# Kernel optimization log

Hardware: AMD Instinct MI355X
Metric: run time of the kernel (lower is better)

## Reference

```python
import jax, jax.numpy as jnp
import numpy as np

B, T, D = 4, 2048, 1024
E, H, K = 8, 2048, 2  # n_expert, expert_dim, top_k


def setup_inputs() -> dict:
    key = jax.random.key(0)
    k1, k2, k3, k4 = jax.random.split(key, 4)
    x = jax.random.normal(k1, (B, T, D), jnp.float32)
    gate_w = jax.random.normal(k2, (D, E), jnp.float32) * 0.02          # Router gate (no bias)
    w1 = jax.random.normal(k3, (E, D, H), jnp.float32) * (1.0 / np.sqrt(D))  # per-expert first Linear
    w2 = jax.random.normal(k4, (E, H, D), jnp.float32) * (1.0 / np.sqrt(H))  # per-expert second Linear
    return {"x": x, "gate_w": gate_w, "w1": w1, "w2": w2}


def reference(x, gate_w, w1, w2):
    b, t, d = x.shape
    xf = x.reshape(-1, d)                                   # [N, D]
    n = xf.shape[0]
    n_expert = gate_w.shape[1]
    # Router
    logits = xf @ gate_w                                    # [N, E]
    probs = jax.nn.softmax(logits, axis=-1)
    topk_probs, topk_idx = jax.lax.top_k(probs, K)          # [N, K]
    topk_probs = topk_probs / jnp.sum(topk_probs, axis=-1, keepdims=True)
    # Dense compute of ALL experts (faithful to original), then gather top-k
    h = jax.nn.gelu(jnp.einsum('nd,edh->neh', xf, w1), approximate=False)  # [N, E, H]
    all_expert_out = jnp.einsum('neh,ehd->ned', h, w2)      # [N, E, D]
    selected = jnp.take_along_axis(all_expert_out, topk_idx[:, :, None], axis=1)  # [N, K, D]
    out = jnp.sum(topk_probs[:, :, None] * selected, axis=1)  # [N, D]  (dropout p=0 -> identity)
    # Load-balancing aux loss
    counts = jnp.zeros((n_expert,), jnp.float32).at[topk_idx.reshape(-1)].add(1.0)
    tokens_per_expert = counts / n
    mean_probs = jnp.mean(probs, axis=0)
    aux_loss = n_expert * jnp.sum(tokens_per_expert * mean_probs)
    return (out.reshape(b, t, d), aux_loss,
            probs.reshape(b, t, n_expert),
            topk_idx.reshape(b, t, K),
            topk_probs.reshape(b, t, K))
```

## Files before the change

### kernel.cpp

```cpp
#include <hip/hip_runtime.h>
#include <hip/hip_bf16.h>
#include <cstdint>

typedef unsigned short u16;
typedef unsigned int u32;
typedef short s16x8 __attribute__((ext_vector_type(8)));
typedef float f32x4 __attribute__((ext_vector_type(4)));

constexpr int NTOK = 8192;
constexpr int DDIM = 1024;
constexpr int NEXP = 8;
constexpr int HDIM = 2048;
constexpr int NPAIR = NTOK * 2;

constexpr size_t OFF_OUT   = 0;
constexpr size_t OFF_AUX   = 8388608;
constexpr size_t OFF_PROBS = 8388609;
constexpr size_t OFF_TIDX  = 8454145;
constexpr size_t OFF_TPR   = 8470529;

constexpr size_t WS_CNT  = 0;
constexpr size_t WS_PSUM = 32;
constexpr size_t WS_BASE = 64;
constexpr size_t WS_IDS  = 1024;
constexpr size_t WS_PRW  = 263168;
constexpr size_t WS_W1T  = 17302528;
constexpr size_t WS_W2T  = 50856960;
constexpr size_t WS_H    = 84411392;
constexpr size_t WS_XG   = 151520256;
constexpr size_t WS_NEED = 185074688;

__device__ __forceinline__ u16 f2b(float f) {
  u32 u = __float_as_uint(f);
  u32 r = (u + 0x7fffu + ((u >> 16) & 1u)) >> 16;
  return (u16)r;
}

typedef const uint32_t __attribute__((address_space(1)))* gptr_t;
typedef uint32_t __attribute__((address_space(3)))* lptr_t;

__device__ __forceinline__ void gload16(const void* gp, void* lp) {
  __builtin_amdgcn_global_load_lds((gptr_t)gp, (lptr_t)(uintptr_t)lp, 16, 0, 0);
}

__global__ __launch_bounds__(256) void tconv_all_kernel(
    const float* __restrict__ w1, u16* __restrict__ w1t,
    const float* __restrict__ w2, u16* __restrict__ w2t) {
  int id = blockIdx.x;
  const float* in;
  u16* out;
  int R, C, e, r;
  if (id < 4096) {
    in = w1; out = w1t; R = DDIM; C = HDIM;
    e = id >> 9; r = id & 511;
  } else {
    id -= 4096;
    in = w2; out = w2t; R = HDIM; C = DDIM;
    e = id >> 9; r = id & 511;
  }
  int xt = (R == DDIM) ? (r & 31) : (r & 15);
  int yt = (R == DDIM) ? (r >> 5) : (r >> 4);
  int c0 = xt * 64, r0 = yt * 64;

  __shared__ float tile[64][65];
  int tx = threadIdx.x & 15, ty = threadIdx.x >> 4;
  const float* src = in + (size_t)e * R * C;
#pragma unroll
  for (int i = 0; i < 4; ++i) {
    int rr = ty + i * 16;
    float4 v = *(const float4*)(src + (size_t)(r0 + rr) * C + c0 + tx * 4);
    tile[rr][tx * 4 + 0] = v.x; tile[rr][tx * 4 + 1] = v.y;
    tile[rr][tx * 4 + 2] = v.z; tile[rr][tx * 4 + 3] = v.w;
  }
  __syncthreads();
  u16* dst = out + (size_t)e * R * C;
#pragma unroll
  for (int i = 0; i < 4; ++i) {
    int c = ty + i * 16;
    ushort4 o;
    o.x = f2b(tile[tx * 4 + 0][c]); o.y = f2b(tile[tx * 4 + 1][c]);
    o.z = f2b(tile[tx * 4 + 2][c]); o.w = f2b(tile[tx * 4 + 3][c]);
    *(ushort4*)(dst + (size_t)(c0 + c) * R + r0 + tx * 4) = o;
  }
}

__global__ __launch_bounds__(256) void router_kernel(
    const float* __restrict__ x, const float* __restrict__ gw,
    float* __restrict__ outbuf,
    int* __restrict__ cnt, float* __restrict__ psum,
    int* __restrict__ ids, float* __restrict__ prw) {
  __shared__ float gwl[DDIM * NEXP];
  __shared__ int lcnt[NEXP];
  __shared__ float psl[NEXP];
  __shared__ int gbl[NEXP];

  const int tid = threadIdx.x;
#pragma unroll
  for (int k = 0; k < 8; ++k)
    ((float4*)gwl)[tid + k * 256] = ((const float4*)gw)[tid + k * 256];
  if (tid < NEXP) { lcnt[tid] = 0; psl[tid] = 0.f; }
  __syncthreads();

  const int tloc = tid >> 2, part = tid & 3;
  const int t = blockIdx.x * 64 + tloc;
  double acc[NEXP];
#pragma unroll
  for (int e = 0; e < NEXP; ++e) acc[e] = 0.0;

  const float* xrow = x + (size_t)t * DDIM + part * 256;
  for (int i = 0; i < 64; ++i) {
    float4 v = ((const float4*)xrow)[i];
    const float* g = &gwl[(part * 256 + i * 4) * NEXP];
#pragma unroll
    for (int j = 0; j < 4; ++j) {
      double xs = (double)((const float*)&v)[j];
#pragma unroll
      for (int e = 0; e < NEXP; ++e) acc[e] += xs * (double)g[j * NEXP + e];
    }
  }
#pragma unroll
  for (int e = 0; e < NEXP; ++e) {
    acc[e] += __shfl_xor(acc[e], 1);
    acc[e] += __shfl_xor(acc[e], 2);
  }

  int e0 = 0, e1 = 0, lp0 = 0, lp1 = 0;
  float tp0 = 0.f, tp1 = 0.f;
  if (part == 0) {
    float l[NEXP];
#pragma unroll
    for (int e = 0; e < NEXP; ++e) l[e] = (float)acc[e];
    float m = l[0];
#pragma unroll
    for (int e = 1; e < NEXP; ++e) m = fmaxf(m, l[e]);
    float p[NEXP], s = 0.f;
#pragma unroll
    for (int e = 0; e < NEXP; ++e) { p[e] = expf(l[e] - m); s += p[e]; }
    float inv = 1.0f / s;
#pragma unroll
    for (int e = 0; e < NEXP; ++e) {
      p[e] *= inv;
      outbuf[OFF_PROBS + (size_t)t * NEXP + e] = p[e];
      atomicAdd(&psl[e], p[e]);
    }
#pragma unroll
    for (int e = 1; e < NEXP; ++e) if (p[e] > p[e0]) e0 = e;
    e1 = -1;
#pragma unroll
    for (int e = 0; e < NEXP; ++e)
      if (e != e0 && (e1 < 0 || p[e] > p[e1])) e1 = e;
    float ps = p[e0] + p[e1];
    tp0 = p[e0] / ps;
    tp1 = p[e1] / ps;
    outbuf[OFF_TIDX + t * 2 + 0] = (float)e0;
    outbuf[OFF_TIDX + t * 2 + 1] = (float)e1;
    outbuf[OFF_TPR + t * 2 + 0] = tp0;
    outbuf[OFF_TPR + t * 2 + 1] = tp1;
    lp0 = atomicAdd(&lcnt[e0], 1);
    lp1 = atomicAdd(&lcnt[e1], 1);
  }
  __syncthreads();
  if (tid < NEXP) {
    gbl[tid] = atomicAdd(&cnt[tid], lcnt[tid]);
    atomicAdd(&psum[tid], psl[tid]);
  }
  __syncthreads();
  if (part == 0) {
    int pos0 = gbl[e0] + lp0;
    int pos1 = gbl[e1] + lp1;
    ids[e0 * NTOK + pos0] = t;
    ids[e1 * NTOK + pos1] = t;
    prw[e0 * NTOK + pos0] = tp0;
    prw[e1 * NTOK + pos1] = tp1;
  }
}

__global__ void finalize_kernel(const int* __restrict__ cnt,
                                const float* __restrict__ psum,
                                int* __restrict__ base, float* __restrict__ outbuf) {
  if (threadIdx.x == 0 && blockIdx.x == 0) {
    int b = 0;
    float aux = 0.f;
    for (int e = 0; e < NEXP; ++e) {
      base[e] = b;
      b += cnt[e];
      aux += (float)cnt[e] * psum[e];
    }
    outbuf[OFF_AUX] = aux * (float)NEXP / ((float)NTOK * (float)NTOK);
  }
}

__global__ __launch_bounds__(256) void gather_kernel(
    const float* __restrict__ x, u16* __restrict__ xg,
    const int* __restrict__ cnt, const int* __restrict__ base,
    const int* __restrict__ ids) {
  const int e = blockIdx.y;
  const int cnte = cnt[e];
  const int lane = threadIdx.x & 31;
  const int rgrp = threadIdx.x >> 5;
#pragma unroll
  for (int p = 0; p < 8; ++p) {
    int pos = blockIdx.x * 64 + p * 8 + rgrp;
    if (pos < cnte) {
      int tok = ids[e * NTOK + pos];
      const float4* src = (const float4*)(x + (size_t)tok * DDIM);
      ushort4* dst = (ushort4*)(xg + (size_t)(base[e] + pos) * DDIM);
#pragma unroll
      for (int pp = 0; pp < 8; ++pp) {
        float4 v = src[pp * 32 + lane];
        ushort4 o;
        o.x = f2b(v.x); o.y = f2b(v.y); o.z = f2b(v.z); o.w = f2b(v.w);
        dst[pp * 32 + lane] = o;
      }
    }
  }
}

template <int MODE>
__global__ __launch_bounds__(256, 3) void moe_gemm_kernel(
    const u16* __restrict__ Asrc, const u16* __restrict__ Bt,
    u16* __restrict__ hout, float* __restrict__ yout,
    const int* __restrict__ cnt, const int* __restrict__ base,
    const int* __restrict__ ids, const float* __restrict__ prw) {
  constexpr int KDIM = (MODE == 0) ? 1024 : 2048;
  constexpr int NDIM = (MODE == 0) ? 2048 : 1024;
  constexpr int NT = KDIM / 32;
  constexpr int NB = NDIM / 128;
  constexpr int MGRP = 4;
  constexpr int QPG = MGRP * NB;
  const int wgid = blockIdx.x;
  const int e = wgid & 7;
  const int q = wgid >> 3;
  const int mg = q / QPG;
  const int r = q % QPG;
  const int m0 = (mg * MGRP + (r % MGRP)) * 128;
  const int n0 = (r / MGRP) * 128;
  const int cnte = cnt[e];
  if (m0 >= cnte) return;
  const int gbase = base[e];

  __shared__ u16 Al[3][128 * 32];
  __shared__ u16 Bl[3][128 * 32];

  const int tid = threadIdx.x;
  const int lane = tid & 63, wid = tid >> 6;
  const int wm = (wid >> 1) * 64, wn = (wid & 1) * 64;
  const int r15 = lane & 15, l4 = lane >> 4;

  const char* aptr[2];
  const char* bptr[2];
#pragma unroll
  for (int qq = 0; qq < 2; ++qq) {
    int j = qq * 256 + tid;
    int row = j >> 2;
    int c = (j & 3) ^ ((row >> 1) & 3);
    int gr = gbase + m0 + row;
    if (gr > NPAIR - 1) gr = NPAIR - 1;
    size_t rowoff = (size_t)gr * KDIM;
    aptr[qq] = (const char*)Asrc + (rowoff + (size_t)c * 8) * 2;
    size_t nrow = (size_t)e * NDIM + n0 + row;
    bptr[qq] = (const char*)Bt + (nrow * KDIM + (size_t)c * 8) * 2;
  }

  f32x4 acc[4][4];
#pragma unroll
  for (int i = 0; i < 4; ++i)
#pragma unroll
    for (int jn = 0; jn < 4; ++jn) acc[i][jn] = (f32x4){0.f, 0.f, 0.f, 0.f};

#define STAGE(b_, kt_)                                                         \
  do {                                                                         \
    const size_t kofs_ = (size_t)(kt_) * 64;               \
    _Pragma("unroll") for (int qq = 0; qq < 2; ++qq) {                         \
      gload16(aptr[qq] + kofs_, (void*)&Al[b_][(size_t)(qq * 256 + tid) * 8]); \
      gload16(bptr[qq] + kofs_, (void*)&Bl[b_][(size_t)(qq * 256 + tid) * 8]); \
    }                                                                          \
  } while (0)

  auto compute = [&](int b) {
    const s16x8* Av = (const s16x8*)Al[b];
    const s16x8* Bv = (const s16x8*)Bl[b];
    s16x8 af[4], bfr[4];
#pragma unroll
    for (int mi = 0; mi < 4; ++mi) {
      int row = wm + mi * 16 + r15;
      af[mi] = Av[row * 4 + (l4 ^ ((row >> 1) & 3))];
    }
#pragma unroll
    for (int ni = 0; ni < 4; ++ni) {
      int row = wn + ni * 16 + r15;
      bfr[ni] = Bv[row * 4 + (l4 ^ ((row >> 1) & 3))];
    }
#pragma unroll
    for (int mi = 0; mi < 4; ++mi)
#pragma unroll
      for (int ni = 0; ni < 4; ++ni)
        acc[mi][ni] = __builtin_amdgcn_mfma_f32_16x16x32_bf16(
            af[mi], bfr[ni], acc[mi][ni], 0, 0, 0);
  };

  STAGE(0, 0);
  STAGE(1, 1);

  int b0 = 0;
  for (int kt = 0; kt < NT; ++kt) {
    if (kt < NT - 1)
      asm volatile("s_waitcnt vmcnt(4)" ::: "memory");
    else
      asm volatile("s_waitcnt vmcnt(0)" ::: "memory");
    __builtin_amdgcn_s_barrier();
    asm volatile("" ::: "memory");
    if (kt + 2 < NT) {
      int bs = b0 + 2; if (bs >= 3) bs -= 3;
      STAGE(bs, kt + 2);
    }
    compute(b0);
    if (++b0 == 3) b0 = 0;
  }
#undef STAGE

#pragma unroll
  for (int mi = 0; mi < 4; ++mi) {
#pragma unroll
    for (int jr = 0; jr < 4; ++jr) {
      int rl = wm + mi * 16 + l4 * 4 + jr;
      if (m0 + rl < cnte) {
        if (MODE == 0) {
          size_t grow = (size_t)(gbase + m0 + rl);
#pragma unroll
          for (int ni = 0; ni < 4; ++ni) {
            float v = acc[mi][ni][jr];
            v = 0.5f * v * (1.0f + erff(v * 0.70710678118654752f));
            int col = n0 + wn + ni * 16 + r15;
            hout[grow * NDIM + col] = f2b(v);
          }
        } else {
          int tok = ids[e * NTOK + m0 + rl];
          float p = prw[e * NTOK + m0 + rl];
#pragma unroll
          for (int ni = 0; ni < 4; ++ni) {
            int col = n0 + wn + ni * 16 + r15;
            atomicAdd(&yout[(size_t)tok * DDIM + col], p * acc[mi][ni][jr]);
          }
        }
      }
    }
  }
}

extern "C" void kernel_launch(void* const* d_in, const int* in_sizes, int n_in,
                              void* d_out, int out_size, void* d_ws, size_t ws_size,
                              hipStream_t stream) {
  const float* x = (const float*)d_in[0];
  const float* gw = (const float*)d_in[1];
  const float* w1 = (const float*)d_in[2];
  const float* w2 = (const float*)d_in[3];
  float* out = (float*)d_out;
  char* w = (char*)d_ws;
  if (ws_size < WS_NEED) return;

  int* cnt = (int*)(w + WS_CNT);
  float* psum = (float*)(w + WS_PSUM);
  int* base = (int*)(w + WS_BASE);
  int* ids = (int*)(w + WS_IDS);
  float* prw = (float*)(w + WS_PRW);
  u16* w1t = (u16*)(w + WS_W1T);
  u16* w2t = (u16*)(w + WS_W2T);
  u16* hbuf = (u16*)(w + WS_H);
  u16* xg = (u16*)(w + WS_XG);

  (void)hipMemsetAsync(w, 0, 96, stream);
  (void)hipMemsetAsync(out + OFF_OUT, 0, (size_t)NTOK * DDIM * sizeof(float), stream);
  router_kernel<<<NTOK / 64, 256, 0, stream>>>(x, gw, out, cnt, psum, ids, prw);
  finalize_kernel<<<1, 64, 0, stream>>>(cnt, psum, base, out);
  gather_kernel<<<dim3(NTOK / 64, NEXP), 256, 0, stream>>>(x, xg, cnt, base, ids);
  tconv_all_kernel<<<8192, 256, 0, stream>>>(w1, w1t, w2, w2t);
  moe_gemm_kernel<0><<<NEXP * 64 * (HDIM / 128), 256, 0, stream>>>(
      xg, w1t, hbuf, nullptr, cnt, base, ids, prw);
  moe_gemm_kernel<1><<<NEXP * 64 * (DDIM / 128), 256, 0, stream>>>(
      hbuf, w2t, nullptr, out + OFF_OUT, cnt, base, ids, prw);
}
```

Before: 333.4 us.

## Enlarge MoE GEMM tiles to 256x256 with 8 waves and interleaved load schedule

```diff
diff --git a/kernel.cpp b/kernel.cpp
--- a/kernel.cpp
+++ b/kernel.cpp
@@ -217,110 +217,145 @@
 }
 
 template <int MODE>
-__global__ __launch_bounds__(256, 3) void moe_gemm_kernel(
+__global__ __launch_bounds__(512, 2) void moe_gemm_kernel(
     const u16* __restrict__ Asrc, const u16* __restrict__ Bt,
     u16* __restrict__ hout, float* __restrict__ yout,
     const int* __restrict__ cnt, const int* __restrict__ base,
     const int* __restrict__ ids, const float* __restrict__ prw) {
   constexpr int KDIM = (MODE == 0) ? 1024 : 2048;
   constexpr int NDIM = (MODE == 0) ? 2048 : 1024;
-  constexpr int NT = KDIM / 32;
-  constexpr int NB = NDIM / 128;
-  constexpr int MGRP = 4;
-  constexpr int QPG = MGRP * NB;
+  constexpr int NT2 = KDIM / 64;
+  constexpr int NITER = NT2 / 2;
+  constexpr int NB = NDIM / 256;
+  constexpr int MGRP = 2, QPG = MGRP * NB;
   const int wgid = blockIdx.x;
   const int e = wgid & 7;
   const int q = wgid >> 3;
   const int mg = q / QPG;
-  const int r = q % QPG;
-  const int m0 = (mg * MGRP + (r % MGRP)) * 128;
-  const int n0 = (r / MGRP) * 128;
+  const int rr_ = q % QPG;
+  const int m0 = (mg * MGRP + (rr_ % MGRP)) * 256;
+  const int n0 = (rr_ / MGRP) * 256;
   const int cnte = cnt[e];
   if (m0 >= cnte) return;
   const int gbase = base[e];
 
-  __shared__ u16 Al[3][128 * 32];
-  __shared__ u16 Bl[3][128 * 32];
+  __shared__ u16 Al[2][256 * 64];
+  __shared__ u16 Bl[2][256 * 64];
 
   const int tid = threadIdx.x;
   const int lane = tid & 63, wid = tid >> 6;
-  const int wm = (wid >> 1) * 64, wn = (wid & 1) * 64;
+  const int wm = (wid >> 2) * 128, wn = (wid & 3) * 64;
   const int r15 = lane & 15, l4 = lane >> 4;
 
-  const char* aptr[2];
-  const char* bptr[2];
-#pragma unroll
-  for (int qq = 0; qq < 2; ++qq) {
-    int j = qq * 256 + tid;
-    int row = j >> 2;
-    int c = (j & 3) ^ ((row >> 1) & 3);
-    int gr = gbase + m0 + row;
-    if (gr > NPAIR - 1) gr = NPAIR - 1;
-    size_t rowoff = (size_t)gr * KDIM;
-    aptr[qq] = (const char*)Asrc + (rowoff + (size_t)c * 8) * 2;
-    size_t nrow = (size_t)e * NDIM + n0 + row;
-    bptr[qq] = (const char*)Bt + (nrow * KDIM + (size_t)c * 8) * 2;
-  }
-
-  f32x4 acc[4][4];
-#pragma unroll
-  for (int i = 0; i < 4; ++i)
+  const char* aS[2][2];
+  const char* bS[2][2];
+  u32 dIx[2][2];
+#pragma unroll
+  for (int h = 0; h < 2; ++h) {
+#pragma unroll
+    for (int qq = 0; qq < 2; ++qq) {
+      int j = qq * 512 + tid;
+      int row128 = j >> 3;
+      int cp = j & 7;
+      int c = cp ^ (row128 & 7);
+      int row = h * 128 + row128;
+      int gr = gbase + m0 + row;
+      if (gr > NPAIR - 1) gr = NPAIR - 1;
+      aS[h][qq] = (const char*)Asrc + ((size_t)gr * KDIM + (size_t)c * 8) * 2;
+      size_t nrow = (size_t)e * NDIM + n0 + row;
+      bS[h][qq] = (const char*)Bt + (nrow * KDIM + (size_t)c * 8) * 2;
+      dIx[h][qq] = (u32)(row * 64 + cp * 8);
+    }
+  }
+
+  f32x4 acc[8][4];
+#pragma unroll
+  for (int i = 0; i < 8; ++i)
 #pragma unroll
     for (int jn = 0; jn < 4; ++jn) acc[i][jn] = (f32x4){0.f, 0.f, 0.f, 0.f};
 
-#define STAGE(b_, kt_)                                                         \
-  do {                                                                         \
-    const size_t kofs_ = (size_t)(kt_) * 64;               \
-    _Pragma("unroll") for (int qq = 0; qq < 2; ++qq) {                         \
-      gload16(aptr[qq] + kofs_, (void*)&Al[b_][(size_t)(qq * 256 + tid) * 8]); \
-      gload16(bptr[qq] + kofs_, (void*)&Bl[b_][(size_t)(qq * 256 + tid) * 8]); \
-    }                                                                          \
+#define STA(bf_, kt_)                                                      \
+  do {                                                                     \
+    _Pragma("unroll") for (int h = 0; h < 2; ++h)                          \
+      _Pragma("unroll") for (int qq = 0; qq < 2; ++qq)                     \
+        gload16(aS[h][qq] + (size_t)(kt_) * 128, (void*)&Al[bf_][dIx[h][qq]]); \
   } while (0)
-
-  auto compute = [&](int b) {
-    const s16x8* Av = (const s16x8*)Al[b];
-    const s16x8* Bv = (const s16x8*)Bl[b];
-    s16x8 af[4], bfr[4];
-#pragma unroll
-    for (int mi = 0; mi < 4; ++mi) {
-      int row = wm + mi * 16 + r15;
-      af[mi] = Av[row * 4 + (l4 ^ ((row >> 1) & 3))];
-    }
-#pragma unroll
-    for (int ni = 0; ni < 4; ++ni) {
-      int row = wn + ni * 16 + r15;
-      bfr[ni] = Bv[row * 4 + (l4 ^ ((row >> 1) & 3))];
-    }
-#pragma unroll
-    for (int mi = 0; mi < 4; ++mi)
-#pragma unroll
-      for (int ni = 0; ni < 4; ++ni)
-        acc[mi][ni] = __builtin_amdgcn_mfma_f32_16x16x32_bf16(
-            af[mi], bfr[ni], acc[mi][ni], 0, 0, 0);
-  };
-
-  STAGE(0, 0);
-  STAGE(1, 1);
-
-  int b0 = 0;
-  for (int kt = 0; kt < NT; ++kt) {
-    if (kt < NT - 1)
-      asm volatile("s_waitcnt vmcnt(4)" ::: "memory");
-    else
-      asm volatile("s_waitcnt vmcnt(0)" ::: "memory");
-    __builtin_amdgcn_s_barrier();
-    asm volatile("" ::: "memory");
-    if (kt + 2 < NT) {
-      int bs = b0 + 2; if (bs >= 3) bs -= 3;
-      STAGE(bs, kt + 2);
-    }
-    compute(b0);
-    if (++b0 == 3) b0 = 0;
-  }
-#undef STAGE
-
-#pragma unroll
-  for (int mi = 0; mi < 4; ++mi) {
+#define STB(bf_, kt_)                                                      \
+  do {                                                                     \
+    _Pragma("unroll") for (int h = 0; h < 2; ++h)                          \
+      _Pragma("unroll") for (int qq = 0; qq < 2; ++qq)                     \
+        gload16(bS[h][qq] + (size_t)(kt_) * 128, (void*)&Bl[bf_][dIx[h][qq]]); \
+  } while (0)
+#define BAR __builtin_amdgcn_s_barrier()
+
+  s16x8 afr[4], bfr[4];
+#define RDA(Av_, mi_, kk_)                                                  \
+  { int row = wm + (mi_) * 16 + r15;                                        \
+    afr[(mi_) & 3] = (Av_)[row * 8 + (((kk_) * 4 + l4) ^ (row & 7))]; }
+#define RDB(Bv_, ni_, kk_)                                                  \
+  { int row = wn + (ni_) * 16 + r15;                                        \
+    bfr[ni_] = (Bv_)[row * 8 + (((kk_) * 4 + l4) ^ (row & 7))]; }
+#define MM16(ML)                                                            \
+  do {                                                                      \
+    __builtin_amdgcn_s_setprio(1);                                          \
+    _Pragma("unroll") for (int mi = 0; mi < 4; ++mi)                        \
+      _Pragma("unroll") for (int ni = 0; ni < 4; ++ni)                      \
+        acc[(ML) + mi][ni] = __builtin_amdgcn_mfma_f32_16x16x32_bf16(       \
+            afr[mi], bfr[ni], acc[(ML) + mi][ni], 0, 0, 0);                 \
+    __builtin_amdgcn_s_setprio(0);                                          \
+  } while (0)
+
+  const s16x8* Av0 = (const s16x8*)Al[0];
+  const s16x8* Bv0 = (const s16x8*)Bl[0];
+  const s16x8* Av1 = (const s16x8*)Al[1];
+  const s16x8* Bv1 = (const s16x8*)Bl[1];
+
+  STA(0, 0); STB(0, 0); STB(1, 1);
+  asm volatile("s_waitcnt vmcnt(4)" ::: "memory");
+  BAR;
+
+  for (int it = 0; it < NITER; ++it) {
+    const bool last = (it == NITER - 1);
+    const int t0 = 2 * it;
+    STA(1, t0 + 1);
+    RDB(Bv0, 0, 0); RDB(Bv0, 1, 0); RDB(Bv0, 2, 0); RDB(Bv0, 3, 0);
+    RDA(Av0, 0, 0); RDA(Av0, 1, 0); RDA(Av0, 2, 0); RDA(Av0, 3, 0);
+    BAR; MM16(0); BAR;
+    RDA(Av0, 4, 0); RDA(Av0, 5, 0); RDA(Av0, 6, 0); RDA(Av0, 7, 0);
+    BAR; MM16(4); BAR;
+    RDB(Bv0, 0, 1); RDB(Bv0, 1, 1); RDB(Bv0, 2, 1); RDB(Bv0, 3, 1);
+    RDA(Av0, 0, 1); RDA(Av0, 1, 1); RDA(Av0, 2, 1); RDA(Av0, 3, 1);
+    BAR; MM16(0); BAR;
+    if (!last) STB(0, t0 + 2);
+    RDA(Av0, 4, 1); RDA(Av0, 5, 1); RDA(Av0, 6, 1); RDA(Av0, 7, 1);
+    BAR; MM16(4);
+    if (last) asm volatile("s_waitcnt vmcnt(0)" ::: "memory");
+    else      asm volatile("s_waitcnt vmcnt(4)" ::: "memory");
+    BAR;
+    if (!last) STA(0, t0 + 2);
+    RDB(Bv1, 0, 0); RDB(Bv1, 1, 0); RDB(Bv1, 2, 0); RDB(Bv1, 3, 0);
+    RDA(Av1, 0, 0); RDA(Av1, 1, 0); RDA(Av1, 2, 0); RDA(Av1, 3, 0);
+    BAR; MM16(0); BAR;
+    RDA(Av1, 4, 0); RDA(Av1, 5, 0); RDA(Av1, 6, 0); RDA(Av1, 7, 0);
+    BAR; MM16(4); BAR;
+    RDB(Bv1, 0, 1); RDB(Bv1, 1, 1); RDB(Bv1, 2, 1); RDB(Bv1, 3, 1);
+    RDA(Av1, 0, 1); RDA(Av1, 1, 1); RDA(Av1, 2, 1); RDA(Av1, 3, 1);
+    BAR; MM16(0); BAR;
+    if (!last) STB(1, t0 + 3);
+    RDA(Av1, 4, 1); RDA(Av1, 5, 1); RDA(Av1, 6, 1); RDA(Av1, 7, 1);
+    BAR; MM16(4);
+    if (!last) asm volatile("s_waitcnt vmcnt(4)" ::: "memory");
+    BAR;
+  }
+#undef STA
+#undef STB
+#undef BAR
+#undef RDA
+#undef RDB
+#undef MM16
+
+#pragma unroll
+  for (int mi = 0; mi < 8; ++mi) {
 #pragma unroll
     for (int jr = 0; jr < 4; ++jr) {
       int rl = wm + mi * 16 + l4 * 4 + jr;
@@ -375,8 +410,8 @@
   finalize_kernel<<<1, 64, 0, stream>>>(cnt, psum, base, out);
   gather_kernel<<<dim3(NTOK / 64, NEXP), 256, 0, stream>>>(x, xg, cnt, base, ids);
   tconv_all_kernel<<<8192, 256, 0, stream>>>(w1, w1t, w2, w2t);
-  moe_gemm_kernel<0><<<NEXP * 64 * (HDIM / 128), 256, 0, stream>>>(
+  moe_gemm_kernel<0><<<NEXP * 32 * (HDIM / 256), 512, 0, stream>>>(
       xg, w1t, hbuf, nullptr, cnt, base, ids, prw);
-  moe_gemm_kernel<1><<<NEXP * 64 * (DDIM / 128), 256, 0, stream>>>(
+  moe_gemm_kernel<1><<<NEXP * 32 * (DDIM / 256), 512, 0, stream>>>(
       hbuf, w2t, nullptr, out + OFF_OUT, cnt, base, ids, prw);
 }
```

Result: slower. 391.7 us (+17.5%).
